# Optimization experiments

Measured on AMD Instinct MI355X. Metric: run time of the kernel, lower is better.

The kernel has to match this reference:

```python
import jax, jax.numpy as jnp
import numpy as np
import jax.scipy.signal as jss

SX, SY, C, K = 256, 256, 3, 10
C0 = [0, 0, 0, 1, 1, 1, 2, 2, 2, 0]
C1 = [[0, 1, 2, 9], [3, 4, 5], [6, 7, 8]]
DD, DT, SIGMA = 5, 0.2, 0.65

_KX = jnp.array([[-1., 0., 1.], [-2., 0., 2.], [-1., 0., 1.]])
_KY = _KX.T


def _conv2(A, Kf):
    # zero-padded 'same' 2D true convolution, vmapped over channel axis
    return jax.vmap(lambda a: jss.convolve2d(a, Kf, mode='same'), in_axes=2, out_axes=2)(A)


def sobel(A):
    # (X, Y, c) -> (X, Y, 2, c): [sobel_y, sobel_x] stacked on axis 2 (FlowLenia convention)
    return jnp.concatenate([_conv2(A, _KY)[:, :, None, :], _conv2(A, _KX)[:, :, None, :]], axis=2)


def growth(U, m, s):
    # bell(U,m,s)*2 - 1
    return jnp.exp(-((U - m) / s) ** 2 / 2.) * 2. - 1.


def get_kernels_fft(R, r, a, w, b):
    # FlowLenia kernel construction: ring distance -> smooth cutoff * sum-of-bumps, normalized, fft2(fftshift)
    mid = SX // 2
    xs = jnp.arange(-mid, mid, dtype=jnp.float32)
    D = jnp.sqrt(xs[:, None] ** 2 + xs[None, :] ** 2)            # (X, Y)
    Dk = D[..., None] / ((R + 15.) * r)                          # (X, Y, k)
    ker = (b * jnp.exp(-(Dk[..., None] - a) ** 2 / w)).sum(-1)   # (X, Y, k)
    sig = 0.5 * (jnp.tanh(-(Dk - 1.) * 10. / 2.) + 1.)           # sigmoid(-(D-1)*10)
    Kk = sig * ker
    nK = Kk / Kk.sum(axis=(0, 1), keepdims=True)
    return jnp.fft.fft2(jnp.fft.fftshift(nK, axes=(0, 1)), axes=(0, 1))


def _rt_apply(A, F):
    # Reintegration tracking with 'wall' border: flow-driven mass redistribution over a (2dd+1)^2 neighborhood
    ii = jnp.arange(SX, dtype=jnp.float32)
    pos = jnp.stack(jnp.meshgrid(ii, ii, indexing='ij'), axis=-1) + 0.5   # (X, Y, 2) cell centers
    ma = DD - SIGMA                                   # max flow magnitude
    mu = pos[..., None] + jnp.clip(DT * F, -ma, ma)   # (X, Y, 2, C) target centers
    mu = jnp.clip(mu, SIGMA, SX - SIGMA)              # wall border
    offs = jnp.arange(-DD, DD + 1)
    gx, gy = jnp.meshgrid(offs, offs, indexing='ij')
    dxs, dys = gx.reshape(-1), gy.reshape(-1)
    clip_hi = min(1., 2. * SIGMA)

    def step(dx, dy):
        Ar = jnp.roll(A, (dx, dy), axis=(0, 1))
        mur = jnp.roll(mu, (dx, dy), axis=(0, 1))
        dpmu = jnp.abs(pos[..., None] - mur)                                  # (X, Y, 2, C)
        sz = 0.5 - dpmu + SIGMA
        area = jnp.prod(jnp.clip(sz, 0., clip_hi), axis=2) / (4. * SIGMA ** 2)  # (X, Y, C)
        return Ar * area

    return jax.vmap(step)(dxs, dys).sum(axis=0)


def setup_inputs() -> dict:
    key = jax.random.key(0)
    ks = jax.random.split(key, 9)
    A = jax.random.uniform(ks[0], (SX, SY, C), dtype=jnp.float32)
    R = jax.random.uniform(ks[1], (), minval=2.0, maxval=25.0)
    r = jax.random.uniform(ks[2], (K,), minval=0.2, maxval=1.0)
    m = jax.random.uniform(ks[3], (K,), minval=0.05, maxval=0.5)
    s = jax.random.uniform(ks[4], (K,), minval=0.001, maxval=0.18)
    h = jax.random.uniform(ks[5], (K,), minval=0.01, maxval=1.0)
    a = jax.random.uniform(ks[6], (K, 3), minval=0.0, maxval=1.0)
    b = jax.random.uniform(ks[7], (K, 3), minval=0.001, maxval=1.0)
    w = jax.random.uniform(ks[8], (K, 3), minval=0.01, maxval=0.5)
    return dict(A=A, R=R, r=r, m=m, s=s, h=h, a=a, b=b, w=w)


def reference(A, R, r, m, s, h, a, b, w):
    fK = get_kernels_fft(R, r, a, w, b)                       # (X, Y, k) complex
    fA = jnp.fft.fft2(A, axes=(0, 1))
    fAk = fA[:, :, jnp.array(C0)]                             # (X, Y, k)
    U = jnp.real(jnp.fft.ifft2(fK * fAk, axes=(0, 1)))        # (X, Y, k)
    U = growth(U, m, s) * h
    U = jnp.dstack([U[:, :, C1[c]].sum(axis=-1) for c in range(C)])  # (X, Y, C)
    nabla_U = sobel(U)                                        # (X, Y, 2, C)
    nabla_A = sobel(A.sum(axis=-1, keepdims=True))            # (X, Y, 2, 1)
    alpha = jnp.clip((A[:, :, None, :] / C) ** 2, 0., 1.)     # (X, Y, 1, C)
    F = nabla_U * (1. - alpha) - nabla_A * alpha              # (X, Y, 2, C)
    return _rt_apply(A, F)
```

## Files before the change

kernel.cpp:

```cpp
#include <hip/hip_runtime.h>

#define NPIX 65536

#define OX1ARE(c) ((0  + (c))*NPIX)
#define OX1AIM(c) ((3  + (c))*NPIX)
#define OX1K(k)   ((6  + (k))*NPIX)
#define OX2ARE(c) ((16 + (c))*NPIX)
#define OX2AIM(c) ((19 + (c))*NPIX)
#define OX2K(k)   ((22 + (k))*NPIX)
#define OX3RE(j)  ((32 + (j))*NPIX)
#define OX3IM(j)  ((37 + (j))*NPIX)
#define OU(k)     ((42 + (k))*NPIX)
#define OROWS     (52*NPIX)

__device__ __forceinline__ void fft256_core(float* __restrict__ re, float* __restrict__ im,
                                            const float* __restrict__ twr,
                                            const float* __restrict__ twi, int lane) {
    #pragma unroll
    for (int s = 1; s <= 8; ++s) {
        int h = 1 << (s - 1);
        #pragma unroll
        for (int b = 0; b < 2; ++b) {
            int idx = b*64 + lane;
            int pos = idx & (h - 1);
            int g   = idx >> (s - 1);
            int i0 = (g << s) + pos;
            int i1 = i0 + h;
            int tj = pos << (8 - s);
            float wr = twr[tj], wi = twi[tj];
            float xr = re[i1], xi = im[i1];
            float br = fmaf(xr, wr, -xi*wi);
            float bi = fmaf(xr, wi,  xi*wr);
            float ar = re[i0], ai = im[i0];
            re[i0] = ar + br; im[i0] = ai + bi;
            re[i1] = ar - br; im[i1] = ai - bi;
        }
    }
}

__device__ __forceinline__ void build_tw(float* twr, float* twi, int t, float sgn) {
    if (t < 128) {
        float ang = (float)t * 0.0245436930f;
        twr[t] = cosf(ang);
        twi[t] = sgn * sinf(ang);
    }
}

__device__ __forceinline__ void store_t4(float* __restrict__ dst, const float* __restrict__ buf,
                                         int off, int t, int lb) {
    float4 v;
    v.x = buf[0*512 + off + t];
    v.y = buf[1*512 + off + t];
    v.z = buf[2*512 + off + t];
    v.w = buf[3*512 + off + t];
    *(float4*)&dst[t*256 + lb] = v;
}

struct KP { float rden, a0,a1,a2, b0,b1,b2, iw0,iw1,iw2; };

__device__ __forceinline__ void load_kp(KP& kp, int k, float R,
        const float* __restrict__ r_, const float* __restrict__ a_,
        const float* __restrict__ b_, const float* __restrict__ w_) {
    kp.rden = 1.0f / ((R + 15.0f) * r_[k]);
    kp.a0 = a_[k*3+0]; kp.a1 = a_[k*3+1]; kp.a2 = a_[k*3+2];
    kp.b0 = b_[k*3+0]; kp.b1 = b_[k*3+1]; kp.b2 = b_[k*3+2];
    kp.iw0 = 1.0f/w_[k*3+0]; kp.iw1 = 1.0f/w_[k*3+1]; kp.iw2 = 1.0f/w_[k*3+2];
}

__device__ __forceinline__ float kval(int di, int dj, const KP& kp) {
    float D  = sqrtf((float)(di*di + dj*dj));
    float Dk = D * kp.rden;
    if (Dk > 3.0f) return 0.0f;
    float d0 = Dk - kp.a0, d1 = Dk - kp.a1, d2 = Dk - kp.a2;
    float ker = kp.b0*expf(-(d0*d0)*kp.iw0)
              + kp.b1*expf(-(d1*d1)*kp.iw1)
              + kp.b2*expf(-(d2*d2)*kp.iw2);
    float sig = 1.0f / (1.0f + expf(10.0f*(Dk - 1.0f)));
    return sig * ker;
}

__global__ __launch_bounds__(256) void fwd_rows(const float* __restrict__ A,
        const float* __restrict__ R_, const float* __restrict__ r_,
        const float* __restrict__ a_, const float* __restrict__ b_,
        const float* __restrict__ w_, float* __restrict__ ws) {
    __shared__ float buf[4*512];
    __shared__ float twr[128], twi[128];
    int p  = blockIdx.x >> 6;
    int lb = (blockIdx.x & 63) * 4;
    int wid = threadIdx.x >> 6, lane = threadIdx.x & 63;
    int t = threadIdx.x;
    build_tw(twr, twi, t, -1.0f);
    int iw = lb + wid;
    float* re = &buf[wid*512];
    float* im = re + 256;

    int fa, fb;
    switch (p) {
        case 0:  fa = 0;  fb = 1;  break;
        case 1:  fa = 2;  fb = 12; break;
        case 2:  fa = 3;  fb = 4;  break;
        case 3:  fa = 5;  fb = 6;  break;
        case 4:  fa = 7;  fb = 8;  break;
        case 5:  fa = 9;  fb = 10; break;
        default: fa = 11; fb = -1; break;
    }
    bool aA = (fa < 3);
    bool bA = (fb >= 0 && fb < 3);
    float R = R_[0];
    int di = ((iw + 128) & 255) - 128;
    KP kpa, kpb;
    if (!aA)      load_kp(kpa, fa - 3, R, r_, a_, b_, w_);
    if (fb >= 3)  load_kp(kpb, fb - 3, R, r_, a_, b_, w_);
    float sum_a = 0.0f, sum_b = 0.0f;
    #pragma unroll
    for (int e = 0; e < 4; ++e) {
        int idx = e*64 + lane;
        int dst = __brev(idx) >> 24;
        int dj  = ((idx + 128) & 255) - 128;
        float vf, vg;
        if (aA) vf = A[(iw*256 + idx)*3 + fa];
        else    { vf = kval(di, dj, kpa); sum_a += vf; }
        if (fb < 0)      vg = 0.0f;
        else if (bA)     vg = A[(iw*256 + idx)*3 + fb];
        else             { vg = kval(di, dj, kpb); sum_b += vg; }
        re[dst] = vf;
        im[dst] = vg;
    }
    if (!aA) {
        float s = sum_a;
        #pragma unroll
        for (int off = 32; off; off >>= 1) s += __shfl_xor(s, off);
        if (lane == 0) ws[OROWS + (fa - 3)*256 + iw] = s;
    }
    if (fb >= 3) {
        float s = sum_b;
        #pragma unroll
        for (int off = 32; off; off >>= 1) s += __shfl_xor(s, off);
        if (lane == 0) ws[OROWS + (fb - 3)*256 + iw] = s;
    }
    __syncthreads();
    fft256_core(re, im, twr, twi, lane);
    __syncthreads();
    if (t <= 128) {
        if (p <= 1) {
            int u2 = (256 - t) & 255;
            float4 Fre, Fim, Gre, Gim;
            float* pF[4] = {&Fre.x, &Fim.x, &Gre.x, &Gim.x};
            #pragma unroll
            for (int l = 0; l < 4; ++l) {
                float zr1 = buf[l*512 + t],  zi1 = buf[l*512 + 256 + t];
                float zr2 = buf[l*512 + u2], zi2 = buf[l*512 + 256 + u2];
                pF[0][l] = 0.5f*(zr1 + zr2);
                pF[1][l] = 0.5f*(zi1 - zi2);
                pF[2][l] = 0.5f*(zi1 + zi2);
                pF[3][l] = 0.5f*(zr2 - zr1);
            }
            if (p == 0) {
                *(float4*)&ws[OX1ARE(0) + t*256 + lb] = Fre;
                *(float4*)&ws[OX1AIM(0) + t*256 + lb] = Fim;
                *(float4*)&ws[OX1ARE(1) + t*256 + lb] = Gre;
                *(float4*)&ws[OX1AIM(1) + t*256 + lb] = Gim;
            } else {
                *(float4*)&ws[OX1ARE(2) + t*256 + lb] = Fre;
                *(float4*)&ws[OX1AIM(2) + t*256 + lb] = Fim;
                *(float4*)&ws[OX1K(9)   + t*256 + lb] = Gre;
            }
        } else {
            float4 va, vb;
            float* pV[2] = {&va.x, &vb.x};
            #pragma unroll
            for (int l = 0; l < 4; ++l) {
                pV[0][l] = buf[l*512 + t];
                pV[1][l] = buf[l*512 + 256 + t];
            }
            *(float4*)&ws[OX1K(fa - 3) + t*256 + lb] = va;
            if (fb >= 0) *(float4*)&ws[OX1K(fb - 3) + t*256 + lb] = vb;
        }
    }
}

__global__ __launch_bounds__(256) void fwd_cols(float* __restrict__ ws) {
    __shared__ float buf[4*512];
    __shared__ float twr[128], twi[128];
    __shared__ float kks[2];
    int bid = blockIdx.x;
    int wid = threadIdx.x >> 6, lane = threadIdx.x & 63;
    int t = threadIdx.x;
    build_tw(twr, twi, t, -1.0f);
    float* re = &buf[wid*512];
    float* im = re + 256;
    if (bid < 99) {
        int c  = bid / 33;
        int ub = (bid % 33) * 4;
        int u  = ub + wid; if (u > 128) u = 128;
        const float* rr = ws + OX1ARE(c) + u*256;
        const float* ri = ws + OX1AIM(c) + u*256;
        #pragma unroll
        for (int e = 0; e < 4; ++e) {
            int idx = e*64 + lane;
            int dst = __brev(idx) >> 24;
            re[dst] = rr[idx];
            im[dst] = ri[idx];
        }
        __syncthreads();
        fft256_core(re, im, twr, twi, lane);
        __syncthreads();
        store_t4(ws + OX2ARE(c), buf, 0,   t, ub);
        store_t4(ws + OX2AIM(c), buf, 256, t, ub);
    } else {
        int q  = (bid - 99) / 33;
        int ub = ((bid - 99) % 33) * 4;
        int u  = ub + wid; if (u > 128) u = 128;
        if (wid < 2) {
            const float* rw = ws + OROWS + (2*q + wid)*256;
            float v = rw[lane] + rw[64+lane] + rw[128+lane] + rw[192+lane];
            #pragma unroll
            for (int off = 32; off; off >>= 1) v += __shfl_xor(v, off);
            if (lane == 0) kks[wid] = 1.0f / (v * 65536.0f);
        }
        const float* ra = ws + OX1K(2*q)     + u*256;
        const float* rb = ws + OX1K(2*q + 1) + u*256;
        #pragma unroll
        for (int e = 0; e < 4; ++e) {
            int idx = e*64 + lane;
            int dst = __brev(idx) >> 24;
            re[dst] = ra[idx];
            im[dst] = rb[idx];
        }
        __syncthreads();
        fft256_core(re, im, twr, twi, lane);
        __syncthreads();
        if (t <= 128) {
            float sa = kks[0], sb = kks[1];
            float4 va, vb;
            va.x = buf[0*512 + t]*sa;  vb.x = buf[0*512 + 256 + t]*sb;
            va.y = buf[1*512 + t]*sa;  vb.y = buf[1*512 + 256 + t]*sb;
            va.z = buf[2*512 + t]*sa;  vb.z = buf[2*512 + 256 + t]*sb;
            va.w = buf[3*512 + t]*sa;  vb.w = buf[3*512 + 256 + t]*sb;
            *(float4*)&ws[OX2K(2*q)     + t*256 + ub] = va;
            *(float4*)&ws[OX2K(2*q + 1) + t*256 + ub] = vb;
        }
    }
}

__global__ __launch_bounds__(256) void inv_rows(float* __restrict__ ws) {
    __shared__ float buf[4*512];
    __shared__ float twr[128], twi[128];
    int j  = blockIdx.x >> 6;
    int lb = (blockIdx.x & 63) * 4;
    int wid = threadIdx.x >> 6, lane = threadIdx.x & 63;
    int t = threadIdx.x;
    build_tw(twr, twi, t, 1.0f);
    int ka = 2*j, kb = 2*j + 1;
    int ca = (ka < 9) ? ka/3 : 0;
    int cb = (kb < 9) ? kb/3 : 0;
    int v  = lb + wid;
    int vr = (256 - v) & 255;
    int vf = (v <= 128) ? v : 256 - v;
    const float* Aare_v = ws + OX2ARE(ca) + v*256;
    const float* Aaim_v = ws + OX2AIM(ca) + v*256;
    const float* Aare_r = ws + OX2ARE(ca) + vr*256;
    const float* Aaim_r = ws + OX2AIM(ca) + vr*256;
    const float* Bare_v = ws + OX2ARE(cb) + v*256;
    const float* Baim_v = ws + OX2AIM(cb) + v*256;
    const float* Bare_r = ws + OX2ARE(cb) + vr*256;
    const float* Baim_r = ws + OX2AIM(cb) + vr*256;
    const float* Ka = ws + OX2K(ka) + vf*256;
    const float* Kb = ws + OX2K(kb) + vf*256;
    float* re = &buf[wid*512];
    float* im = re + 256;
    #pragma unroll
    for (int e = 0; e < 4; ++e) {
        int idx = e*64 + lane;
        int dst = __brev(idx) >> 24;
        bool hi = idx > 128;
        int uf = hi ? 256 - idx : idx;
        const float* pAr = hi ? Aare_r : Aare_v;
        const float* pAi = hi ? Aaim_r : Aaim_v;
        const float* pBr = hi ? Bare_r : Bare_v;
        const float* pBi = hi ? Baim_r : Baim_v;
        float ar = pAr[uf];
        float ai = pAi[uf]; ai = hi ? -ai : ai;
        float br = pBr[uf];
        float bi = pBi[uf]; bi = hi ? -bi : bi;
        float kva = Ka[uf], kvb = Kb[uf];
        float uar = ar*kva, uai = ai*kva;
        float ubr = br*kvb, ubi = bi*kvb;
        re[dst] = uar - ubi;
        im[dst] = uai + ubr;
    }
    __syncthreads();
    fft256_core(re, im, twr, twi, lane);
    __syncthreads();
    store_t4(ws + OX3RE(j), buf, 0,   t, lb);
    store_t4(ws + OX3IM(j), buf, 256, t, lb);
}

__global__ __launch_bounds__(256) void inv_cols(float* __restrict__ ws,
                                                const float* __restrict__ m_,
                                                const float* __restrict__ s_,
                                                const float* __restrict__ h_,
                                                float* __restrict__ out) {
    __shared__ float buf[4*512];
    __shared__ float twr[128], twi[128];
    int j  = blockIdx.x >> 6;
    int lb = (blockIdx.x & 63) * 4;
    int wid = threadIdx.x >> 6, lane = threadIdx.x & 63;
    int t = threadIdx.x;
    build_tw(twr, twi, t, 1.0f);
    {
        int gid = blockIdx.x * 256 + t;
        if (gid < 49152) ((float4*)out)[gid] = make_float4(0.f, 0.f, 0.f, 0.f);
    }
    float* re = &buf[wid*512];
    float* im = re + 256;
    const float* rr = ws + OX3RE(j) + (lb + wid)*256;
    const float* ri = ws + OX3IM(j) + (lb + wid)*256;
    #pragma unroll
    for (int e = 0; e < 4; ++e) {
        int idx = e*64 + lane;
        int dst = __brev(idx) >> 24;
        re[dst] = rr[idx];
        im[dst] = ri[idx];
    }
    __syncthreads();
    fft256_core(re, im, twr, twi, lane);
    __syncthreads();
    int k0 = 2*j, k1 = 2*j + 1;
    float m0 = m_[k0], m1 = m_[k1];
    float c0 = 0.5f/(s_[k0]*s_[k0]), c1 = 0.5f/(s_[k1]*s_[k1]);
    float h0 = h_[k0], h1 = h_[k1];
    float4 va, vb;
    #pragma unroll
    for (int l = 0; l < 4; ++l) {
        float u0 = buf[l*512 + t]       - m0;
        float u1 = buf[l*512 + 256 + t] - m1;
        (&va.x)[l] = h0 * fmaf(2.0f, expf(-(u0*u0)*c0), -1.0f);
        (&vb.x)[l] = h1 * fmaf(2.0f, expf(-(u1*u1)*c1), -1.0f);
    }
    *(float4*)&ws[OU(k0) + t*256 + lb] = va;
    *(float4*)&ws[OU(k1) + t*256 + lb] = vb;
}

__global__ __launch_bounds__(256) void growth_scatter(const float* __restrict__ A,
                                                      const float* __restrict__ ws,
                                                      float* __restrict__ out) {
    __shared__ float Gs[3][256];
    __shared__ float As[3][256];
    int b = blockIdx.x;
    int c = b >> 8;
    int x = b & 255;
    int t = threadIdx.x;
    int nk = (c == 0) ? 4 : 3;
    #pragma unroll
    for (int rr = 0; rr < 3; ++rr) {
        int xr = x - 1 + rr;
        float sv = 0.0f, gv = 0.0f;
        if (xr >= 0 && xr <= 255) {
            int idx = xr*256 + t;
            int base = idx*3;
            sv = A[base] + A[base + 1] + A[base + 2];
            for (int kk = 0; kk < nk; ++kk) {
                int k = (kk == 3) ? 9 : c*3 + kk;
                gv += ws[OU(k) + idx];
            }
        }
        As[rr][t] = sv;
        Gs[rr][t] = gv;
    }
    __syncthreads();
    int y = t;
    float vA[3][3], vU[3][3];
    #pragma unroll
    for (int ii = 0; ii < 3; ++ii)
        #pragma unroll
        for (int jj = 0; jj < 3; ++jj) {
            int yy = y - 1 + jj;
            bool ok = (yy >= 0 && yy <= 255);
            vA[ii][jj] = ok ? As[ii][yy] : 0.0f;
            vU[ii][jj] = ok ? Gs[ii][yy] : 0.0f;
        }
    float gyA = (vA[0][0] + 2.0f*vA[0][1] + vA[0][2]) - (vA[2][0] + 2.0f*vA[2][1] + vA[2][2]);
    float gxA = (vA[0][0] + 2.0f*vA[1][0] + vA[2][0]) - (vA[0][2] + 2.0f*vA[1][2] + vA[2][2]);
    float gy  = (vU[0][0] + 2.0f*vU[0][1] + vU[0][2]) - (vU[2][0] + 2.0f*vU[2][1] + vU[2][2]);
    float gx  = (vU[0][0] + 2.0f*vU[1][0] + vU[2][0]) - (vU[0][2] + 2.0f*vU[1][2] + vU[2][2]);
    float a = A[(x*256 + y)*3 + c];
    float al = (a / 3.0f); al = al * al;
    al = fminf(fmaxf(al, 0.0f), 1.0f);
    float F0 = gy * (1.0f - al) - gyA * al;
    float F1 = gx * (1.0f - al) - gxA * al;
    float d0 = fminf(fmaxf(0.2f * F0, -4.35f), 4.35f);
    float d1 = fminf(fmaxf(0.2f * F1, -4.35f), 4.35f);
    float mux = fminf(fmaxf((float)x + 0.5f + d0, 0.65f), 255.35f);
    float muy = fminf(fmaxf((float)y + 0.5f + d1, 0.65f), 255.35f);
    float dxp = mux - ((float)x + 0.5f);
    float dyp = muy - ((float)y + 0.5f);
    int bx = (int)ceilf(dxp - 1.15f);
    int by = (int)ceilf(dyp - 1.15f);
    float wx[3], wy[3];
    #pragma unroll
    for (int q = 0; q < 3; ++q) {
        wx[q] = __builtin_amdgcn_fmed3f(1.15f - fabsf((float)(bx + q) - dxp), 0.0f, 1.0f);
        wy[q] = __builtin_amdgcn_fmed3f(1.15f - fabsf((float)(by + q) - dyp), 0.0f, 1.0f);
    }
    float am = a * (1.0f / (4.0f * 0.65f * 0.65f));
    #pragma unroll
    for (int qx = 0; qx < 3; ++qx) {
        float wxa = am * wx[qx];
        if (wxa == 0.0f) continue;
        int xd = (x + bx + qx) & 255;
        #pragma unroll
        for (int qy = 0; qy < 3; ++qy) {
            float wgt = wxa * wy[qy];
            if (wgt != 0.0f) {
                int yd = (y + by + qy) & 255;
                atomicAdd(&out[(xd*256 + yd)*3 + c], wgt);
            }
        }
    }
}

extern "C" void kernel_launch(void* const* d_in, const int* in_sizes, int n_in,
                              void* d_out, int out_size, void* d_ws, size_t ws_size,
                              hipStream_t stream) {
    const float* A = (const float*)d_in[0];
    const float* R = (const float*)d_in[1];
    const float* r = (const float*)d_in[2];
    const float* m = (const float*)d_in[3];
    const float* s = (const float*)d_in[4];
    const float* h = (const float*)d_in[5];
    const float* a = (const float*)d_in[6];
    const float* b = (const float*)d_in[7];
    const float* w = (const float*)d_in[8];
    float* ws  = (float*)d_ws;
    float* out = (float*)d_out;

    fwd_rows<<<7*64, 256, 0, stream>>>(A, R, r, a, b, w, ws);
    fwd_cols<<<99 + 165, 256, 0, stream>>>(ws);
    inv_rows<<<5*64, 256, 0, stream>>>(ws);
    inv_cols<<<5*64, 256, 0, stream>>>(ws, m, s, h, out);
    growth_scatter<<<768, 256, 0, stream>>>(A, ws, out);
}
```

Baseline: 117.3 us.

## Replace global atomic scatter with per-row gather into shared-memory accumulator

The fused growth/scatter kernel is split in two. The first writes each cell's mass, x-displacement and target y-center into a packed workspace. A new kernel then gives each output row to one block, which gathers contributions from the 11 source rows within the displacement range and accumulates y-spread weights with shared-memory atomics before writing each output once. This removes global atomics and the separate zeroing of the output, at the cost of an extra launch, an extra workspace round trip, and 11x redundant reads of the packed data.

```diff
diff --git a/kernel.cpp b/kernel.cpp
--- a/kernel.cpp
+++ b/kernel.cpp
@@ -11,7 +11,8 @@
 #define OX3RE(j)  ((32 + (j))*NPIX)
 #define OX3IM(j)  ((37 + (j))*NPIX)
 #define OU(k)     ((42 + (k))*NPIX)
-#define OROWS     (52*NPIX)
+#define OPACK(c)  ((52 + 4*(c))*NPIX)
+#define OROWS     (64*NPIX)
 
 __device__ __forceinline__ void fft256_core(float* __restrict__ re, float* __restrict__ im,
                                             const float* __restrict__ twr,
@@ -299,8 +300,7 @@
 __global__ __launch_bounds__(256) void inv_cols(float* __restrict__ ws,
                                                 const float* __restrict__ m_,
                                                 const float* __restrict__ s_,
-                                                const float* __restrict__ h_,
-                                                float* __restrict__ out) {
+                                                const float* __restrict__ h_) {
     __shared__ float buf[4*512];
     __shared__ float twr[128], twi[128];
     int j  = blockIdx.x >> 6;
@@ -308,10 +308,6 @@
     int wid = threadIdx.x >> 6, lane = threadIdx.x & 63;
     int t = threadIdx.x;
     build_tw(twr, twi, t, 1.0f);
-    {
-        int gid = blockIdx.x * 256 + t;
-        if (gid < 49152) ((float4*)out)[gid] = make_float4(0.f, 0.f, 0.f, 0.f);
-    }
     float* re = &buf[wid*512];
     float* im = re + 256;
     const float* rr = ws + OX3RE(j) + (lb + wid)*256;
@@ -342,9 +338,8 @@
     *(float4*)&ws[OU(k1) + t*256 + lb] = vb;
 }
 
-__global__ __launch_bounds__(256) void growth_scatter(const float* __restrict__ A,
-                                                      const float* __restrict__ ws,
-                                                      float* __restrict__ out) {
+__global__ __launch_bounds__(256) void growth_mu(const float* __restrict__ A,
+                                                 float* __restrict__ ws) {
     __shared__ float Gs[3][256];
     __shared__ float As[3][256];
     int b = blockIdx.x;
@@ -393,31 +388,44 @@
     float d1 = fminf(fmaxf(0.2f * F1, -4.35f), 4.35f);
     float mux = fminf(fmaxf((float)x + 0.5f + d0, 0.65f), 255.35f);
     float muy = fminf(fmaxf((float)y + 0.5f + d1, 0.65f), 255.35f);
-    float dxp = mux - ((float)x + 0.5f);
-    float dyp = muy - ((float)y + 0.5f);
-    int bx = (int)ceilf(dxp - 1.15f);
-    int by = (int)ceilf(dyp - 1.15f);
-    float wx[3], wy[3];
-    #pragma unroll
-    for (int q = 0; q < 3; ++q) {
-        wx[q] = __builtin_amdgcn_fmed3f(1.15f - fabsf((float)(bx + q) - dxp), 0.0f, 1.0f);
-        wy[q] = __builtin_amdgcn_fmed3f(1.15f - fabsf((float)(by + q) - dyp), 0.0f, 1.0f);
-    }
-    float am = a * (1.0f / (4.0f * 0.65f * 0.65f));
-    #pragma unroll
-    for (int qx = 0; qx < 3; ++qx) {
-        float wxa = am * wx[qx];
-        if (wxa == 0.0f) continue;
-        int xd = (x + bx + qx) & 255;
-        #pragma unroll
-        for (int qy = 0; qy < 3; ++qy) {
-            float wgt = wxa * wy[qy];
-            if (wgt != 0.0f) {
-                int yd = (y + by + qy) & 255;
-                atomicAdd(&out[(xd*256 + yd)*3 + c], wgt);
+    float4 pk;
+    pk.x = a;
+    pk.y = mux - ((float)x + 0.5f);
+    pk.z = muy;
+    pk.w = 0.0f;
+    *(float4*)&ws[OPACK(c) + (x*256 + y)*4] = pk;
+}
+
+__global__ __launch_bounds__(256) void rt_scatter(const float* __restrict__ ws,
+                                                  float* __restrict__ out) {
+    __shared__ float acc[256];
+    int b = blockIdx.x;
+    int c = b >> 8;
+    int x = b & 255;
+    int t = threadIdx.x;
+    acc[t] = 0.0f;
+    __syncthreads();
+    const float4* pp = (const float4*)&ws[OPACK(c)];
+    #pragma unroll
+    for (int i = 0; i < 11; ++i) {
+        int s = i - 5;
+        int xs = (x - s) & 255;
+        float dxf = (float)(x - xs);
+        float4 v = pp[xs*256 + t];
+        float wx = __builtin_amdgcn_fmed3f(1.15f - fabsf(dxf - v.y), 0.0f, 1.0f);
+        float wxa = v.x * wx;
+        if (wxa != 0.0f) {
+            int by = (int)ceilf(v.z - 1.65f);
+            float fy = (float)by + 0.5f - v.z;
+            #pragma unroll
+            for (int q = 0; q < 3; ++q) {
+                float ay = __builtin_amdgcn_fmed3f(1.15f - fabsf(fy + (float)q), 0.0f, 1.0f);
+                atomicAdd(&acc[(by + q) & 255], wxa * ay);
             }
         }
     }
+    __syncthreads();
+    out[(x*256 + t)*3 + c] = acc[t] * (1.0f / (4.0f * 0.65f * 0.65f));
 }
 
 extern "C" void kernel_launch(void* const* d_in, const int* in_sizes, int n_in,
@@ -438,6 +446,7 @@
     fwd_rows<<<7*64, 256, 0, stream>>>(A, R, r, a, b, w, ws);
     fwd_cols<<<99 + 165, 256, 0, stream>>>(ws);
     inv_rows<<<5*64, 256, 0, stream>>>(ws);
-    inv_cols<<<5*64, 256, 0, stream>>>(ws, m, s, h, out);
-    growth_scatter<<<768, 256, 0, stream>>>(A, ws, out);
-}
+    inv_cols<<<5*64, 256, 0, stream>>>(ws, m, s, h);
+    growth_mu<<<768, 256, 0, stream>>>(A, ws);
+    rt_scatter<<<768, 256, 0, stream>>>(ws, out);
+}
```

Measured after the change: 113.7 us. 1.03x faster.
